# Kernel optimization log

Measured on AMD Instinct MI355X. Metric: run time of the kernel, lower is better.

## Reference

```python
import jax, jax.numpy as jnp
import numpy as np

K = 7      # number of neighbor volumes (init k)
PS = 7     # patch size (unfold.ps / wpsum.ps)
WS = 13    # search window side -> O = WS*WS candidates per query
WR = WS // 2
EPS = 1e-6


def setup_inputs() -> dict:
    key = jax.random.key(0)
    k1, k2, k3, k4 = jax.random.split(key, 4)
    C, E, H, W = 64, 32, 128, 128
    return {
        "x": jax.random.normal(k1, (C, H, W), jnp.float32),
        "xe": jax.random.normal(k2, (E, H, W), jnp.float32),
        "ye": jax.random.normal(k3, (E, H, W), jnp.float32),
        "log_temp": 0.1 * jax.random.normal(k4, (1, H, W), jnp.float32),
    }


def _box_sum(img, ps):
    # img: [B, H, W] -> centered ps x ps box sum with zero padding, same shape
    kern = jnp.ones((1, 1, ps, ps), img.dtype)
    return jax.lax.conv_general_dilated(img[:, None], kern, (1, 1), "SAME")[:, 0]


def _forward(x, xe, ye, log_temp):
    C, H, W_ = x.shape
    E = xe.shape[0]
    offs = np.stack(np.meshgrid(np.arange(WS), np.arange(WS), indexing="ij"), -1).reshape(-1, 2)
    O = offs.shape[0]
    dis = jnp.asarray(offs[:, 0]); djs = jnp.asarray(offs[:, 1])

    xe_pad = jnp.pad(xe, ((0, 0), (WR, WR), (WR, WR)))
    x_pad = jnp.pad(x, ((0, 0), (WR, WR), (WR, WR)))

    # ---- search: per-candidate patch SSD between query/database embeddings ----
    def per_off_dist(di, dj):
        xs = jax.lax.dynamic_slice(xe_pad, (0, di, dj), (E, H, W_))
        return jnp.sum((ye - xs) ** 2, axis=0)  # [H, W] pixel-wise sq dist

    diff2 = jax.vmap(per_off_dist)(dis, djs)        # [O, H, W]
    dists = -_box_sum(diff2, PS)                    # patch SSD, negated

    # ---- temperature: avgpool of log_temp over the ps x ps patch (avgpool=True) ----
    lt = _box_sum(log_temp, PS) / float(PS * PS)    # [1, H, W]
    temp = jnp.exp(lt)                              # temp_bias=1 -> log bias 0

    # ---- NeuralNearestNeighbors: k rounds of temp-softmax with exclusion ----
    logits = dists / temp                           # [O, H, W]
    Ws = []
    for _ in range(K):  # small structural loop over k neighbor volumes
        w = jax.nn.softmax(logits, axis=0)
        Ws.append(w)
        logits = logits + jnp.log(jnp.clip(1.0 - w, EPS))
    Wk = jnp.stack(Ws, 0)                           # [K, O, H, W]

    # ---- wpsum + fold fused: for stride-1 centered patches the patch offset
    # cancels, so out[k,c,y] = sum_o boxsum_ps(W[k,o])[y] * x[c, y + off(o)] ----
    Wsum = _box_sum(Wk.reshape(K * O, H, W_), PS).reshape(K, O, H, W_)
    Wsum_o = jnp.moveaxis(Wsum, 1, 0)               # [O, K, H, W]

    def body(out, inp):
        di, dj, wso = inp
        xs = jax.lax.dynamic_slice(x_pad, (0, di, dj), (C, H, W_))
        return out + wso[:, None] * xs[None], None  # [K, C, H, W]

    out0 = jnp.zeros((K, C, H, W_), x.dtype)
    out, _ = jax.lax.scan(body, out0, (dis, djs, Wsum_o))
    return out.reshape(K * C, H, W_)


def reference(x, xe, ye, log_temp):
    return _forward(x, xe, ye, log_temp)
```

## Files before the change

kernel.cpp:

```cpp
#include <hip/hip_runtime.h>
#include <hip/hip_bf16.h>
#include <hip/hip_fp16.h>

#define HW 16384

using u16 = unsigned short;
using u32 = unsigned int;
typedef __attribute__((ext_vector_type(2))) float f32x2;

__device__ __forceinline__ u16 f2h(float f) {
    __half h = __float2half(f);
    return __builtin_bit_cast(u16, h);
}
__device__ __forceinline__ void dot2acc(float& acc, u32 a, u32 b) {
    asm("v_dot2_f32_f16 %0, %1, %2, %0" : "+v"(acc) : "v"(a), "v"(b));
}
__device__ __forceinline__ u32 hadd2u(u32 a, u32 b) {
    __half2 r = __hadd2(__builtin_bit_cast(__half2, a), __builtin_bit_cast(__half2, b));
    return __builtin_bit_cast(u32, r);
}
__device__ __forceinline__ u32 hsub2u(u32 a, u32 b) {
    __half2 r = __hsub2(__builtin_bit_cast(__half2, a), __builtin_bit_cast(__half2, b));
    return __builtin_bit_cast(u32, r);
}
#define SELLO 0x05040100u
#define SELHI 0x07060302u

__global__ __launch_bounds__(256) void k_prep(
        const float* __restrict__ x, const float* __restrict__ xe,
        const float* __restrict__ ye,
        u16* __restrict__ xh, float* __restrict__ xeT,
        float* __restrict__ yeT, float* __restrict__ nx2, float* __restrict__ ny) {
    __shared__ float s_px[4][64], s_py[4][64];
    int tid = threadIdx.x;
    int g = tid >> 6, l = tid & 63;
    int y = blockIdx.x * 64 + l;

#pragma unroll
    for (int j = 0; j < 16; j++) {
        int c = g * 16 + j;
        xh[c * HW + y] = f2h(x[c * HW + y]);
    }

    float sx = 0.f, sy = 0.f;
#pragma unroll
    for (int e0 = 0; e0 < 8; e0 += 4) {
        int e = g * 8 + e0;
        float4 v = make_float4(xe[(e + 0) * HW + y], xe[(e + 1) * HW + y],
                               xe[(e + 2) * HW + y], xe[(e + 3) * HW + y]);
        *reinterpret_cast<float4*>(xeT + y * 32 + e) = v;
        sx += v.x * v.x + v.y * v.y + v.z * v.z + v.w * v.w;
        float4 u = make_float4(ye[(e + 0) * HW + y], ye[(e + 1) * HW + y],
                               ye[(e + 2) * HW + y], ye[(e + 3) * HW + y]);
        *reinterpret_cast<float4*>(yeT + y * 32 + e) = u;
        sy += u.x * u.x + u.y * u.y + u.z * u.z + u.w * u.w;
    }
    s_px[g][l] = sx;
    s_py[g][l] = sy;
    __syncthreads();
    if (tid < 64) {
        nx2[y] = s_px[0][l] + s_px[1][l];
        nx2[HW + y] = s_px[2][l] + s_px[3][l];
        ny[y] = s_py[0][l] + s_py[1][l] + s_py[2][l] + s_py[3][l];
    }
}

__global__ __launch_bounds__(256) void k_norms(
        const float* __restrict__ ny, const float* __restrict__ lt,
        float2* __restrict__ st) {
    int y = blockIdx.x * 256 + threadIdx.x;
    int py = y >> 7, px = y & 127;
    float s = 0.f, t = 0.f;
    for (int dy = -3; dy <= 3; dy++)
        for (int dx = -3; dx <= 3; dx++) {
            int yy = py + dy, xx = px + dx;
            if ((unsigned)yy < 128u && (unsigned)xx < 128u) {
                int p = yy * 128 + xx;
                s += ny[p];
                t += lt[p];
            }
        }
    float tinv = __expf(-t * (1.0f / 49.0f));
    st[y] = make_float2(tinv, tinv * s);
}

__global__ __launch_bounds__(1024) void k_logits(
        const float* __restrict__ xeT, const float* __restrict__ yeT,
        const float* __restrict__ nx2, float* __restrict__ lg) {
#pragma clang fp contract(fast)
    __shared__ __align__(16) char arena[78320];
    float* s_xe = (float*)arena;
    float* s_nx = (float*)(arena + 47872);
    float* s_d2 = (float*)(arena + 50864);
    float* s_hs = (float*)arena;

    int di = blockIdx.x;
    int tile = blockIdx.y;
    int h = blockIdx.z;
    int h0 = (tile >> 3) * 16, w0 = (tile & 7) * 16;
    int gr0 = h0 + di - 9, gc0 = w0 - 9;
    int tid = threadIdx.x;

    for (int idx = tid; idx < 748 * 4; idx += 1024) {
        int cell = idx >> 2, q = idx & 3;
        int r = cell / 34, c = cell - r * 34;
        int gy = gr0 + r, gx = gc0 + c;
        float4 v = make_float4(0.f, 0.f, 0.f, 0.f);
        if ((unsigned)gy < 128u && (unsigned)gx < 128u)
            v = *reinterpret_cast<const float4*>(
                    xeT + (size_t)(gy * 128 + gx) * 32 + h * 16 + q * 4);
        *reinterpret_cast<float4*>(s_xe + cell * 16 + ((q ^ (cell & 3)) << 2)) = v;
    }
    for (int idx = tid; idx < 748; idx += 1024) {
        int r = idx / 34, c = idx - r * 34;
        int gy = gr0 + r, gx = gc0 + c;
        float v = 0.f;
        if ((unsigned)gy < 128u && (unsigned)gx < 128u)
            v = nx2[h * HW + gy * 128 + gx];
        s_nx[idx] = v;
    }
    __syncthreads();

    if (tid < 484) {
        int zr = tid / 22, zc = tid - zr * 22;
        int gy = h0 - 3 + zr, gx = w0 - 3 + zc;
        bool zin = ((unsigned)gy < 128u) && ((unsigned)gx < 128u);
        f32x2 yv[8];
#pragma unroll
        for (int j = 0; j < 8; j++) yv[j] = (f32x2){0.f, 0.f};
        if (zin) {
            const float* yp = yeT + (size_t)(gy * 128 + gx) * 32 + h * 16;
#pragma unroll
            for (int j = 0; j < 4; j++) {
                float4 t = *reinterpret_cast<const float4*>(yp + j * 4);
                yv[2 * j] = (f32x2){t.x, t.y};
                yv[2 * j + 1] = (f32x2){t.z, t.w};
            }
        }
        int cell0 = zr * 34 + zc;
#pragma unroll
        for (int dj = 0; dj < 13; dj++) {
            int cell = cell0 + dj;
            const float* bp = s_xe + cell * 16;
            int sw = cell & 3;
            f32x2 a0 = {0.f, 0.f}, a1 = {0.f, 0.f};
#pragma unroll
            for (int q = 0; q < 4; q++) {
                float4 xv = *reinterpret_cast<const float4*>(bp + ((q ^ sw) << 2));
                a0 += ((f32x2){xv.x, xv.y}) * yv[2 * q];
                a1 += ((f32x2){xv.z, xv.w}) * yv[2 * q + 1];
            }
            float cr = a0.x + a0.y + a1.x + a1.y;
            float d2v = fmaf(-2.f, cr, s_nx[cell]);
            s_d2[dj * 528 + zr * 24 + zc] = zin ? d2v : 0.f;
        }
    }
    __syncthreads();

    for (int idx = tid; idx < 1144; idx += 1024) {
        int dj = idx / 88, rem = idx - dj * 88;
        int r = rem >> 2, c4 = (rem & 3) * 4;
        const float* p = s_d2 + dj * 528 + r * 24 + c4;
        float4 pa = *reinterpret_cast<const float4*>(p);
        float4 pb = *reinterpret_cast<const float4*>(p + 4);
        float4 pc = *reinterpret_cast<const float4*>(p + 8);
        float h0s = pa.x + pa.y + pa.z + pa.w + pb.x + pb.y + pb.z;
        float h1s = h0s - pa.x + pb.w;
        float h2s = h1s - pa.y + pc.x;
        float h3s = h2s - pa.z + pc.y;
        *reinterpret_cast<float4*>(s_hs + (dj * 22 + r) * 16 + c4) =
            make_float4(h0s, h1s, h2s, h3s);
    }
    __syncthreads();

    for (int idx = tid; idx < 832; idx += 1024) {
        int dj = idx >> 6, rem = idx & 63;
        int i = rem >> 2, j4 = (rem & 3) * 4;
        const float* p = s_hs + (dj * 22 + i) * 16 + j4;
        float4 s = *reinterpret_cast<const float4*>(p);
#pragma unroll
        for (int d = 1; d < 7; d++) {
            float4 t = *reinterpret_cast<const float4*>(p + d * 16);
            s.x += t.x; s.y += t.y; s.z += t.z; s.w += t.w;
        }
        int y = (h0 + i) * 128 + (w0 + j4);
        *reinterpret_cast<float4*>(
            lg + ((size_t)h * 169 + di * 13 + dj) * HW + y) = s;
    }
}

__global__ __launch_bounds__(256) void k_softmax(
        const float* __restrict__ lg, const float2* __restrict__ st,
        u16* __restrict__ Wkt) {
    __shared__ float s_lg[169 * 34];
    int tid = threadIdx.x;
    int y0 = blockIdx.x * 32;
    for (int idx = tid; idx < 169 * 32; idx += 256) {
        int o = idx >> 5, p = idx & 31;
        s_lg[o * 34 + p] = lg[(size_t)o * HW + y0 + p]
                         + lg[(size_t)(169 + o) * HW + y0 + p];
    }
    __syncthreads();
    int pix = tid >> 3, t = tid & 7;
    int y = y0 + pix;
    float2 ab = st[y];
    float l[22];
#pragma unroll
    for (int j = 0; j < 22; j++) {
        int o = t + 8 * j;
        l[j] = (o < 169) ? -fmaf(ab.x, s_lg[o * 34 + pix], ab.y) : -3e38f;
    }
    u32 wp0[22], wp1[22], wp2[22], wp3[22];
#pragma unroll
    for (int j = 0; j < 22; j++) { wp0[j] = 0u; wp1[j] = 0u; wp2[j] = 0u; wp3[j] = 0u; }

    float e[22];
#pragma unroll
    for (int k = 0; k < 7; k++) {
        float m = -3e38f;
#pragma unroll
        for (int j = 0; j < 22; j++) m = fmaxf(m, l[j]);
        m = fmaxf(m, __shfl_xor(m, 1));
        m = fmaxf(m, __shfl_xor(m, 2));
        m = fmaxf(m, __shfl_xor(m, 4));
        float s = 0.f;
#pragma unroll
        for (int j = 0; j < 22; j++) { e[j] = __expf(l[j] - m); s += e[j]; }
        s += __shfl_xor(s, 1);
        s += __shfl_xor(s, 2);
        s += __shfl_xor(s, 4);
        float rs = 1.0f / s;
#pragma unroll
        for (int j = 0; j < 22; j++) {
            float w = e[j] * rs;
            u32 hh = (u32)f2h(w);
            if (k == 0) wp0[j] |= hh;
            else if (k == 1) wp0[j] |= hh << 16;
            else if (k == 2) wp1[j] |= hh;
            else if (k == 3) wp1[j] |= hh << 16;
            else if (k == 4) wp2[j] |= hh;
            else if (k == 5) wp2[j] |= hh << 16;
            else wp3[j] |= hh;
            if (k < 6) l[j] += __logf(fmaxf(1.0f - w, 1e-6f));
        }
    }
#pragma unroll
    for (int j = 0; j < 22; j++) {
        int o = t + 8 * j;
        if (o < 169)
            *reinterpret_cast<uint4*>(Wkt + ((size_t)o * HW + y) * 8) =
                make_uint4(wp0[j], wp1[j], wp2[j], wp3[j]);
    }
}

__global__ __launch_bounds__(256) void k_wsum(
        const u16* __restrict__ Wkt, u32* __restrict__ WsP) {
    __shared__ u16 s_w[38 * 39 * 8];
    __shared__ u16 s_v[32 * 38 * 8];
    int o2 = blockIdx.x;
    int di = o2 / 7, djp = o2 - di * 7;
    int oA = di * 13 + 2 * djp;
    bool hasB = (djp < 6);
    int tile = blockIdx.y;
    int h0 = (tile >> 2) * 32, w0 = (tile & 3) * 32;
    int tid = threadIdx.x;

    auto stage = [&](int o) {
        const u16* src = Wkt + (size_t)o * (HW * 8);
        for (int idx = tid; idx < 38 * 38; idx += 256) {
            int r = idx / 38, c = idx - r * 38;
            int gy = h0 - 3 + r, gx = w0 - 3 + c;
            uint4 v = make_uint4(0u, 0u, 0u, 0u);
            if ((unsigned)gy < 128u && (unsigned)gx < 128u)
                v = *reinterpret_cast<const uint4*>(src + (gy * 128 + gx) * 8);
            *reinterpret_cast<uint4*>(s_w + (r * 39 + c) * 8) = v;
        }
    };
    auto vert = [&]() {
        for (int u = tid; u < 304; u += 256) {
            int g = u / 38, c = u - g * 38;
            int r0 = g * 4;
            uint4 q[10];
#pragma unroll
            for (int d = 0; d < 10; d++)
                q[d] = *reinterpret_cast<const uint4*>(s_w + ((r0 + d) * 39 + c) * 8);
            uint4 s = q[0];
#pragma unroll
            for (int d = 1; d < 7; d++) {
                s.x = hadd2u(s.x, q[d].x); s.y = hadd2u(s.y, q[d].y);
                s.z = hadd2u(s.z, q[d].z); s.w = hadd2u(s.w, q[d].w);
            }
            *reinterpret_cast<uint4*>(s_v + (r0 * 38 + c) * 8) = s;
#pragma unroll
            for (int j = 1; j < 4; j++) {
                s.x = hadd2u(hsub2u(s.x, q[j - 1].x), q[j + 6].x);
                s.y = hadd2u(hsub2u(s.y, q[j - 1].y), q[j + 6].y);
                s.z = hadd2u(hsub2u(s.z, q[j - 1].z), q[j + 6].z);
                s.w = hadd2u(hsub2u(s.w, q[j - 1].w), q[j + 6].w);
                *reinterpret_cast<uint4*>(s_v + ((r0 + j) * 38 + c) * 8) = s;
            }
        }
    };
    auto horiz = [&](uint4 (&rr)[4]) {
#pragma unroll
        for (int i = 0; i < 4; i++) {
            int u = tid + i * 256;
            int r = u >> 5, cx = u & 31;
            __half2 s0 = __builtin_bit_cast(__half2, 0u);
            __half2 s1 = s0, s2 = s0, s3 = s0;
#pragma unroll
            for (int d = 0; d < 7; d++) {
                uint4 q = *reinterpret_cast<const uint4*>(s_v + (r * 38 + cx + d) * 8);
                s0 = __hadd2(s0, __builtin_bit_cast(__half2, q.x));
                s1 = __hadd2(s1, __builtin_bit_cast(__half2, q.y));
                s2 = __hadd2(s2, __builtin_bit_cast(__half2, q.z));
                s3 = __hadd2(s3, __builtin_bit_cast(__half2, q.w));
            }
            rr[i] = make_uint4(
                __builtin_bit_cast(u32, s0), __builtin_bit_cast(u32, s1),
                __builtin_bit_cast(u32, s2), __builtin_bit_cast(u32, s3));
        }
    };

    uint4 rA[4], rB[4];
#pragma unroll
    for (int i = 0; i < 4; i++) rB[i] = make_uint4(0u, 0u, 0u, 0u);

    stage(oA);
    __syncthreads();
    vert();
    __syncthreads();
    horiz(rA);
    if (hasB) {
        __syncthreads();
        stage(oA + 1);
        __syncthreads();
        vert();
        __syncthreads();
        horiz(rB);
    }

#pragma unroll
    for (int i = 0; i < 4; i++) {
        int u = tid + i * 256;
        int r = u >> 5, cx = u & 31;
        int y = (h0 + r) * 128 + (w0 + cx);
        u32* dst = WsP + ((size_t)o2 * HW + y) * 8;
        uint4 lo = make_uint4(
            __builtin_amdgcn_perm(rB[i].x, rA[i].x, SELLO),
            __builtin_amdgcn_perm(rB[i].x, rA[i].x, SELHI),
            __builtin_amdgcn_perm(rB[i].y, rA[i].y, SELLO),
            __builtin_amdgcn_perm(rB[i].y, rA[i].y, SELHI));
        uint4 hi = make_uint4(
            __builtin_amdgcn_perm(rB[i].z, rA[i].z, SELLO),
            __builtin_amdgcn_perm(rB[i].z, rA[i].z, SELHI),
            __builtin_amdgcn_perm(rB[i].w, rA[i].w, SELLO),
            0u);
        *reinterpret_cast<uint4*>(dst) = lo;
        *reinterpret_cast<uint4*>(dst + 4) = hi;
    }
}

__global__ __launch_bounds__(512, 2) void k_agg(
        const u16* __restrict__ xh, const u32* __restrict__ WsP,
        float* __restrict__ out) {
    __shared__ u16 s_x[64 * 16 * 32];
    int tb = blockIdx.x;
    int h0 = (tb >> 3) * 4, w0 = (tb & 7) * 16;
    int tid = threadIdx.x;

#pragma unroll
    for (int i = 0; i < 8; i++) {
        int it = tid + i * 512;
        int ch = it >> 6;
        int r = (it >> 2) & 15;
        int c0 = (it & 3) * 8;
        int gy = h0 - 6 + r, gx0 = w0 - 6 + c0;
        uint4 v = make_uint4(0u, 0u, 0u, 0u);
        if ((unsigned)gy < 128u) {
            const u16* src = xh + (size_t)ch * HW + gy * 128;
            if (gx0 >= 0 && gx0 <= 120) {
                v = *reinterpret_cast<const uint4*>(src + gx0);
            } else {
                auto pk = [&](int gx) -> u32 {
                    u32 lo = ((unsigned)gx < 128u) ? (u32)src[gx] : 0u;
                    u32 hi = ((unsigned)(gx + 1) < 128u) ? (u32)src[gx + 1] : 0u;
                    return lo | (hi << 16);
                };
                v = make_uint4(pk(gx0), pk(gx0 + 2), pk(gx0 + 4), pk(gx0 + 6));
            }
        }
        *reinterpret_cast<uint4*>(s_x + (ch * 16 + r) * 32 + c0) = v;
    }
    __syncthreads();

    int cc = tid >> 6, pix = tid & 63;
    int pr = pix >> 4, pc = pix & 15;
    int y = (h0 + pr) * 128 + (w0 + pc);
    const u32* wsrc = WsP + (size_t)y * 8;
    const u32* s_x32 = reinterpret_cast<const u32*>(s_x);
    u32 sh = (u32)(pc & 1) * 16;
    int base0 = cc * 8 * 256 + (pc >> 1);

    float acc[7][8];
#pragma unroll
    for (int k = 0; k < 7; k++)
#pragma unroll
        for (int q = 0; q < 8; q++) acc[k][q] = 0.f;

    auto loadW = [&](int di, uint4 (&A)[7], uint4 (&B)[7]) {
        const u32* wdi = wsrc + (size_t)(di * 7) * (HW * 8);
#pragma unroll
        for (int djp = 0; djp < 7; djp++) {
            const u32* wp = wdi + (size_t)djp * (HW * 8);
            A[djp] = *reinterpret_cast<const uint4*>(wp);
            B[djp] = *reinterpret_cast<const uint4*>(wp + 4);
        }
    };
    auto compute = [&](int di, const uint4 (&A)[7], const uint4 (&B)[7]) {
        int rowoff = (pr + di) * 16;
#pragma unroll
        for (int q = 0; q < 8; q++) {
            const u32* p = s_x32 + base0 + q * 256 + rowoff;
            u32 f0 = p[0], f1 = p[1], f2 = p[2], f3 = p[3];
            u32 f4 = p[4], f5 = p[5], f6 = p[6], f7 = p[7];
            u32 x2;
            x2 = __builtin_amdgcn_alignbit(f1, f0, sh);
            dot2acc(acc[0][q], A[0].x, x2); dot2acc(acc[1][q], A[0].y, x2);
            dot2acc(acc[2][q], A[0].z, x2); dot2acc(acc[3][q], A[0].w, x2);
            dot2acc(acc[4][q], B[0].x, x2); dot2acc(acc[5][q], B[0].y, x2);
            dot2acc(acc[6][q], B[0].z, x2);
            x2 = __builtin_amdgcn_alignbit(f2, f1, sh);
            dot2acc(acc[0][q], A[1].x, x2); dot2acc(acc[1][q], A[1].y, x2);
            dot2acc(acc[2][q], A[1].z, x2); dot2acc(acc[3][q], A[1].w, x2);
            dot2acc(acc[4][q], B[1].x, x2); dot2acc(acc[5][q], B[1].y, x2);
            dot2acc(acc[6][q], B[1].z, x2);
            x2 = __builtin_amdgcn_alignbit(f3, f2, sh);
            dot2acc(acc[0][q], A[2].x, x2); dot2acc(acc[1][q], A[2].y, x2);
            dot2acc(acc[2][q], A[2].z, x2); dot2acc(acc[3][q], A[2].w, x2);
            dot2acc(acc[4][q], B[2].x, x2); dot2acc(acc[5][q], B[2].y, x2);
            dot2acc(acc[6][q], B[2].z, x2);
            x2 = __builtin_amdgcn_alignbit(f4, f3, sh);
            dot2acc(acc[0][q], A[3].x, x2); dot2acc(acc[1][q], A[3].y, x2);
            dot2acc(acc[2][q], A[3].z, x2); dot2acc(acc[3][q], A[3].w, x2);
            dot2acc(acc[4][q], B[3].x, x2); dot2acc(acc[5][q], B[3].y, x2);
            dot2acc(acc[6][q], B[3].z, x2);
            x2 = __builtin_amdgcn_alignbit(f5, f4, sh);
            dot2acc(acc[0][q], A[4].x, x2); dot2acc(acc[1][q], A[4].y, x2);
            dot2acc(acc[2][q], A[4].z, x2); dot2acc(acc[3][q], A[4].w, x2);
            dot2acc(acc[4][q], B[4].x, x2); dot2acc(acc[5][q], B[4].y, x2);
            dot2acc(acc[6][q], B[4].z, x2);
            x2 = __builtin_amdgcn_alignbit(f6, f5, sh);
            dot2acc(acc[0][q], A[5].x, x2); dot2acc(acc[1][q], A[5].y, x2);
            dot2acc(acc[2][q], A[5].z, x2); dot2acc(acc[3][q], A[5].w, x2);
            dot2acc(acc[4][q], B[5].x, x2); dot2acc(acc[5][q], B[5].y, x2);
            dot2acc(acc[6][q], B[5].z, x2);
            x2 = __builtin_amdgcn_alignbit(f7, f6, sh);
            dot2acc(acc[0][q], A[6].x, x2); dot2acc(acc[1][q], A[6].y, x2);
            dot2acc(acc[2][q], A[6].z, x2); dot2acc(acc[3][q], A[6].w, x2);
            dot2acc(acc[4][q], B[6].x, x2); dot2acc(acc[5][q], B[6].y, x2);
            dot2acc(acc[6][q], B[6].z, x2);
        }
    };

    uint4 WA[7], WB[7], WC[7], WD[7];
    loadW(0, WA, WB);
#pragma unroll 1
    for (int di = 0; di < 12; di += 2) {
        loadW(di + 1, WC, WD);
        compute(di, WA, WB);
        loadW(di + 2, WA, WB);
        compute(di + 1, WC, WD);
    }
    compute(12, WA, WB);

#pragma unroll
    for (int k = 0; k < 7; k++)
#pragma unroll
        for (int q = 0; q < 8; q++)
            out[(k * 64 + cc * 8 + q) * HW + y] = acc[k][q];
}

extern "C" void kernel_launch(void* const* d_in, const int* in_sizes, int n_in,
                              void* d_out, int out_size, void* d_ws, size_t ws_size,
                              hipStream_t stream) {
    (void)in_sizes; (void)n_in; (void)out_size; (void)ws_size;
    const float* x  = (const float*)d_in[0];
    const float* xe = (const float*)d_in[1];
    const float* ye = (const float*)d_in[2];
    const float* lt = (const float*)d_in[3];
    float* out = (float*)d_out;
    char* ws = (char*)d_ws;

    u16*    xh  = (u16*)(ws + 0);
    float*  xeT = (float*)(ws + 2097152u);
    float*  yeT = (float*)(ws + 4194304u);
    u16*    Wkt = (u16*)(ws + 6291456u);
    float*  lg  = (float*)(ws + 50593792u);
    u32*    WsP = (u32*)(ws + 72744960u);
    float*  nx2 = (float*)(ws + 120455168u);
    float*  ny  = (float*)(ws + 120586240u);
    float2* st  = (float2*)(ws + 120651776u);

    k_prep<<<256, 256, 0, stream>>>(x, xe, ye, xh, xeT, yeT, nx2, ny);
    k_norms<<<64, 256, 0, stream>>>(ny, lt, st);
    k_logits<<<dim3(13, 64, 2), 1024, 0, stream>>>(xeT, yeT, nx2, lg);
    k_softmax<<<512, 256, 0, stream>>>(lg, st, Wkt);
    k_wsum<<<dim3(91, 16), 256, 0, stream>>>(Wkt, WsP);
    k_agg<<<256, 512, 0, stream>>>(xh, WsP, out);
}
```

Baseline: 133.1 us.

## Fuse temperature/norm prep into softmax and remap block order for XCD locality

```diff
diff --git a/kernel.cpp b/kernel.cpp
--- a/kernel.cpp
+++ b/kernel.cpp
@@ -63,25 +63,6 @@
         nx2[HW + y] = s_px[2][l] + s_px[3][l];
         ny[y] = s_py[0][l] + s_py[1][l] + s_py[2][l] + s_py[3][l];
     }
-}
-
-__global__ __launch_bounds__(256) void k_norms(
-        const float* __restrict__ ny, const float* __restrict__ lt,
-        float2* __restrict__ st) {
-    int y = blockIdx.x * 256 + threadIdx.x;
-    int py = y >> 7, px = y & 127;
-    float s = 0.f, t = 0.f;
-    for (int dy = -3; dy <= 3; dy++)
-        for (int dx = -3; dx <= 3; dx++) {
-            int yy = py + dy, xx = px + dx;
-            if ((unsigned)yy < 128u && (unsigned)xx < 128u) {
-                int p = yy * 128 + xx;
-                s += ny[p];
-                t += lt[p];
-            }
-        }
-    float tinv = __expf(-t * (1.0f / 49.0f));
-    st[y] = make_float2(tinv, tinv * s);
 }
 
 __global__ __launch_bounds__(1024) void k_logits(
@@ -190,11 +171,38 @@
 }
 
 __global__ __launch_bounds__(256) void k_softmax(
-        const float* __restrict__ lg, const float2* __restrict__ st,
-        u16* __restrict__ Wkt) {
+        const float* __restrict__ lg, const float* __restrict__ ny,
+        const float* __restrict__ lt, u16* __restrict__ Wkt) {
     __shared__ float s_lg[169 * 34];
+    __shared__ float2 s_ab[32];
     int tid = threadIdx.x;
-    int y0 = blockIdx.x * 32;
+    int lbid = blockIdx.x;
+    int cls = lbid & 7, i0 = lbid >> 3;
+    int t2 = cls + 8 * (i0 & 1);
+    int rr = i0 >> 1;
+    int tr = t2 >> 2, q = t2 & 3;
+    int r = tr * 32 + rr;
+    int y0 = r * 128 + q * 32;
+
+    if (tid < 32) {
+        int px = q * 32 + tid;
+        float s = 0.f, t = 0.f;
+        for (int dy = -3; dy <= 3; dy++) {
+            int yy = r + dy;
+            if ((unsigned)yy < 128u) {
+                for (int dx = -3; dx <= 3; dx++) {
+                    int xx = px + dx;
+                    if ((unsigned)xx < 128u) {
+                        int p = yy * 128 + xx;
+                        s += ny[p];
+                        t += lt[p];
+                    }
+                }
+            }
+        }
+        float tinv = __expf(-t * (1.0f / 49.0f));
+        s_ab[tid] = make_float2(tinv, tinv * s);
+    }
     for (int idx = tid; idx < 169 * 32; idx += 256) {
         int o = idx >> 5, p = idx & 31;
         s_lg[o * 34 + p] = lg[(size_t)o * HW + y0 + p]
@@ -203,7 +211,7 @@
     __syncthreads();
     int pix = tid >> 3, t = tid & 7;
     int y = y0 + pix;
-    float2 ab = st[y];
+    float2 ab = s_ab[pix];
     float l[22];
 #pragma unroll
     for (int j = 0; j < 22; j++) {
@@ -257,11 +265,11 @@
         const u16* __restrict__ Wkt, u32* __restrict__ WsP) {
     __shared__ u16 s_w[38 * 39 * 8];
     __shared__ u16 s_v[32 * 38 * 8];
-    int o2 = blockIdx.x;
+    int o2 = blockIdx.y;
     int di = o2 / 7, djp = o2 - di * 7;
     int oA = di * 13 + 2 * djp;
     bool hasB = (djp < 6);
-    int tile = blockIdx.y;
+    int tile = blockIdx.x;
     int h0 = (tile >> 2) * 32, w0 = (tile & 3) * 32;
     int tid = threadIdx.x;
 
@@ -365,7 +373,12 @@
         const u16* __restrict__ xh, const u32* __restrict__ WsP,
         float* __restrict__ out) {
     __shared__ u16 s_x[64 * 16 * 32];
-    int tb = blockIdx.x;
+    int lbid = blockIdx.x;
+    int cls = lbid & 7, idx0 = lbid >> 3;
+    int t2 = cls + 8 * (idx0 & 1);
+    int j = idx0 >> 1;
+    int tr = t2 >> 2, tc2 = t2 & 3;
+    int tb = ((tr << 3) + (j >> 1)) * 8 + (tc2 * 2 + (j & 1));
     int h0 = (tb >> 3) * 4, w0 = (tb & 7) * 16;
     int tid = threadIdx.x;
 
@@ -500,12 +513,10 @@
     u32*    WsP = (u32*)(ws + 72744960u);
     float*  nx2 = (float*)(ws + 120455168u);
     float*  ny  = (float*)(ws + 120586240u);
-    float2* st  = (float2*)(ws + 120651776u);
 
     k_prep<<<256, 256, 0, stream>>>(x, xe, ye, xh, xeT, yeT, nx2, ny);
-    k_norms<<<64, 256, 0, stream>>>(ny, lt, st);
     k_logits<<<dim3(13, 64, 2), 1024, 0, stream>>>(xeT, yeT, nx2, lg);
-    k_softmax<<<512, 256, 0, stream>>>(lg, st, Wkt);
-    k_wsum<<<dim3(91, 16), 256, 0, stream>>>(Wkt, WsP);
+    k_softmax<<<512, 256, 0, stream>>>(lg, ny, lt, Wkt);
+    k_wsum<<<dim3(16, 91), 256, 0, stream>>>(Wkt, WsP);
     k_agg<<<256, 512, 0, stream>>>(xh, WsP, out);
 }
```

Measured after the change: 131.7 us. About the same (-1.1%).
